# Performance work log

Hardware: AMD Instinct MI355X
Metric: run time of the kernel (lower is better)

## Reference

```python
import jax, jax.numpy as jnp
import numpy as np

EPS = 1e-5
N0 = 2000  # number of crystals


def batchnorm(x, gamma, beta):
    # training-mode BatchNorm1d over rows (biased variance, like torch normalization)
    mu = jnp.mean(x, axis=0)
    var = jnp.mean(jnp.square(x - mu), axis=0)
    return (x - mu) * jax.lax.rsqrt(var + EPS) * gamma + beta


def setup_inputs() -> dict:
    key = jax.random.key(0)
    ks = jax.random.split(key, 16)
    N, M, F, B = 100000, 12, 64, 41
    d = {
        "atom_fea": jax.random.normal(ks[0], (N, 92), jnp.float32),
        "nbr_fea": jax.random.uniform(ks[1], (N, M, B), jnp.float32),
        "nbr_fea_idx": jax.random.randint(ks[2], (N, M), 0, N),
        "crystal_atom_idx": jnp.sort(jax.random.randint(ks[3], (N,), 0, N0)),
        "emb_w": jax.random.normal(ks[4], (92, F), jnp.float32) * 0.1,
        "emb_b": jax.random.normal(ks[5], (F,), jnp.float32) * 0.1,
        "conv_w": jax.random.normal(ks[6], (3, 2 * F + B, 2 * F), jnp.float32) * 0.05,
        "conv_b": jax.random.normal(ks[7], (3, 2 * F), jnp.float32) * 0.05,
        "bn1_g": jnp.ones((3, 2 * F), jnp.float32),
        "bn1_b": jnp.zeros((3, 2 * F), jnp.float32),
        "bn2_g": jnp.ones((3, F), jnp.float32),
        "bn2_b": jnp.zeros((3, F), jnp.float32),
        "fc_w": jax.random.normal(ks[8], (F, 128), jnp.float32) * 0.1,
        "fc_b": jax.random.normal(ks[9], (128,), jnp.float32) * 0.1,
        "head_w": jax.random.normal(ks[10], (128, 256), jnp.float32) * 0.1,
        "head_b": jax.random.normal(ks[11], (256,), jnp.float32) * 0.1,
        "out_w": jax.random.normal(ks[12], (256, 1), jnp.float32) * 0.1,
        "out_b": jax.random.normal(ks[13], (1,), jnp.float32) * 0.1,
    }
    return d


def reference(atom_fea, nbr_fea, nbr_fea_idx, crystal_atom_idx,
              emb_w, emb_b, conv_w, conv_b, bn1_g, bn1_b, bn2_g, bn2_b,
              fc_w, fc_b, head_w, head_b, out_w, out_b):
    N, M = nbr_fea_idx.shape
    F = emb_w.shape[1]
    x = atom_fea @ emb_w + emb_b  # (N, F)
    for i in range(conv_w.shape[0]):
        nbr_atom = x[nbr_fea_idx]  # (N, M, F) gather
        self_fea = jnp.broadcast_to(x[:, None, :], (N, M, F))
        tot = jnp.concatenate([self_fea, nbr_atom, nbr_fea], axis=2)  # (N, M, 2F+B)
        g = jnp.einsum('nmc,cf->nmf', tot, conv_w[i]) + conv_b[i]  # (N, M, 2F)
        g = batchnorm(g.reshape(N * M, 2 * F), bn1_g[i], bn1_b[i]).reshape(N, M, 2 * F)
        nbr_filter = jax.nn.sigmoid(g[:, :, :F])
        nbr_core = jax.nn.softplus(g[:, :, F:])
        nbr_sumed = jnp.sum(nbr_filter * nbr_core, axis=1)  # (N, F)
        nbr_sumed = batchnorm(nbr_sumed, bn2_g[i], bn2_b[i])
        x = jax.nn.softplus(x + nbr_sumed)
    # mean-pool atoms into crystals
    seg = crystal_atom_idx
    sums = jax.ops.segment_sum(x, seg, num_segments=N0)
    cnts = jax.ops.segment_sum(jnp.ones((N,), x.dtype), seg, num_segments=N0)
    crys = sums / jnp.maximum(cnts, 1.0)[:, None]  # (N0, F)
    crys = jax.nn.relu(crys @ fc_w + fc_b)
    h = crys @ head_w + head_b
    out = h @ out_w + out_b
    return out
```

## Files before the change

### kernel.cpp

```cpp
#include <hip/hip_runtime.h>
#include <hip/hip_bf16.h>

#define NATOM 100000
#define MNBR  12
#define FDIM  64
#define BDIM  41
#define C2    128
#define EPSBN 1e-5f
#define NEDGE (NATOM * MNBR)
#define KP48  48
#define NFRAG  16384
#define NFRAGS 8192

typedef __attribute__((ext_vector_type(8))) short bf16x8;
typedef __attribute__((ext_vector_type(4))) unsigned short u16x4;
typedef __attribute__((ext_vector_type(4))) float f32x4;

#define X_OFF    0L
#define XB_OFF   6400000L
#define S_OFF    9600000L
#define NBRB_OFF 16000000L
#define AS_OFF   54400000L
#define BALL_OFF 60800000L
#define BALLS_OFF 60808192L
#define BN1S_OFF 60812288L
#define BN2S_OFF 60828672L
#define SC1_OFF  60836864L
#define SH1_OFF  60836992L
#define SC2_OFF  60837120L
#define SH2_OFF  60837184L
#define CRY_OFF  60837248L
#define CNT_OFF  60965248L
#define ZB_OFF   60967296L
#define WS_NEED_FUSED ((ZB_OFF + 76800000L) * 4L)
#define ZERO_OFF BN1S_OFF
#define ZERO_CNT 154960L

__device__ __forceinline__ float bf2f(unsigned short u) {
    return __uint_as_float(((unsigned)u) << 16);
}
__device__ __forceinline__ unsigned short f2bf(float f) {
    __hip_bfloat16 h = __float2bfloat16(f);
    return *(unsigned short*)&h;
}
__device__ __forceinline__ float softplus_f(float v) {
    return fmaxf(v, 0.f) + __logf(1.f + __expf(-fabsf(v)));
}

__global__ void k_zero(float* __restrict__ p, long cnt) {
    long i = (long)blockIdx.x * 256 + threadIdx.x;
    if (i < cnt) p[i] = 0.f;
}

__global__ void k_nbrcvt(const float* __restrict__ nbr, __hip_bfloat16* __restrict__ outb) {
    long i = (long)blockIdx.x * 256 + threadIdx.x;
    if (i >= (long)NEDGE * 6) return;
    long e = i / 6;
    int c = (int)(i - e * 6);
    const float* src = nbr + e * BDIM + c * 8;
    bf16x8 v;
#pragma unroll
    for (int j = 0; j < 8; ++j) {
        int k = c * 8 + j;
        float f = (k < BDIM) ? src[j] : 0.f;
        v[j] = (short)f2bf(f);
    }
    *(bf16x8*)((short*)outb + e * KP48 + c * 8) = v;
}

__global__ void k_bcvt(const float* __restrict__ cw, __hip_bfloat16* __restrict__ ballf,
                       __hip_bfloat16* __restrict__ ballfS) {
    int i = blockIdx.x * 256 + threadIdx.x;
    if (i < NFRAG) {
        int T = i / 2048, r = i - T * 2048;
        int lidx = (r >> 3) & 63, e = i & 7;
        int s4 = r >> 9;
        int lo = lidx & 15, hi = lidx >> 4;
        int krow = 64 + s4 * 32 + hi * 8 + e;
        float v = (krow < 169) ? cw[krow * C2 + T * 16 + lo] : 0.f;
        ballf[i] = __float2bfloat16(v);
    } else if (i < NFRAG + NFRAGS) {
        int i2 = i - NFRAG;
        int T = i2 / 1024, r = i2 - T * 1024;
        int lidx = (r >> 3) & 63, e = i2 & 7;
        int s = r >> 9;
        int lo = lidx & 15, hi = lidx >> 4;
        int krow = s * 32 + hi * 8 + e;
        ballfS[i2] = __float2bfloat16(cw[krow * C2 + T * 16 + lo]);
    }
}

__global__ __launch_bounds__(256)
void k_embed(const float* __restrict__ af, const float* __restrict__ ew,
             const float* __restrict__ eb, float* __restrict__ x,
             __hip_bfloat16* __restrict__ xb) {
    int t = threadIdx.x;
    int c = t & 63, ag = t >> 6;
    long n0 = (long)blockIdx.x * 16 + ag * 4;
    float acc[4] = {0.f, 0.f, 0.f, 0.f};
    for (int k4 = 0; k4 < 23; ++k4) {
        float w0 = ew[(4 * k4 + 0) * FDIM + c];
        float w1 = ew[(4 * k4 + 1) * FDIM + c];
        float w2 = ew[(4 * k4 + 2) * FDIM + c];
        float w3 = ew[(4 * k4 + 3) * FDIM + c];
#pragma unroll
        for (int a = 0; a < 4; ++a) {
            const float4* ar = (const float4*)(af + (n0 + a) * 92);
            float4 v = ar[k4];
            acc[a] += v.x * w0 + v.y * w1 + v.z * w2 + v.w * w3;
        }
    }
    float b = eb[c];
#pragma unroll
    for (int a = 0; a < 4; ++a) {
        float v = acc[a] + b;
        x[(n0 + a) * FDIM + c] = v;
        xb[(n0 + a) * FDIM + c] = __float2bfloat16(v);
    }
}

__global__ __launch_bounds__(256, 8)
void k_lin(const __hip_bfloat16* __restrict__ xb, const __hip_bfloat16* __restrict__ ballfS,
           __hip_bfloat16* __restrict__ aS) {
    int t = threadIdx.x, w = t >> 6, l = t & 63;
    int lo = l & 15, hi = l >> 4;
    long atom0 = ((long)blockIdx.x * 4 + w) * 16;
    if (atom0 >= NATOM) return;
    const short* xs = (const short*)xb + (atom0 + lo) * FDIM + hi * 8;
    bf16x8 A0 = *(const bf16x8*)(xs);
    bf16x8 A1 = *(const bf16x8*)(xs + 32);
    const short* bS = (const short*)ballfS;
#pragma unroll
    for (int T = 0; T < 8; ++T) {
        bf16x8 B0 = *(const bf16x8*)(bS + T * 1024 + l * 8);
        bf16x8 B1 = *(const bf16x8*)(bS + T * 1024 + 512 + l * 8);
        f32x4 z = {0.f, 0.f, 0.f, 0.f};
        z = __builtin_amdgcn_mfma_f32_16x16x32_bf16(A0, B0, z, 0, 0, 0);
        z = __builtin_amdgcn_mfma_f32_16x16x32_bf16(A1, B1, z, 0, 0, 0);
#pragma unroll
        for (int qq = 0; qq < 4; ++qq)
            aS[(atom0 + hi * 4 + qq) * C2 + T * 16 + lo] = __float2bfloat16(z[qq]);
    }
}

__global__ __launch_bounds__(256, 4)
void k_edge_dense(const __hip_bfloat16* __restrict__ xb,
                  const __hip_bfloat16* __restrict__ nbrb,
                  const __hip_bfloat16* __restrict__ ballf,
                  const __hip_bfloat16* __restrict__ aS,
                  const int* __restrict__ idxp,
                  float* __restrict__ bn1_slots,
                  __hip_bfloat16* __restrict__ zb) {
    __shared__ float bn_s[256];
    const int t = threadIdx.x;
    const int w = t >> 6, l = t & 63;
    const int lo = l & 15, hi = l >> 4;
    const short* xbS = (const short*)xb;
    const short* nbS = (const short*)nbrb;
    const short* aSS = (const short*)aS;
    const short* bb  = (const short*)ballf;
    short* zbS = (short*)zb;

    bn_s[t] = 0.f;
    __syncthreads();

    const long tile0 = (long)blockIdx.x * 8 + w * 2;
    const bf16x8 zz = {0, 0, 0, 0, 0, 0, 0, 0};
    const int off1 = (hi < 2) ? (32 + hi * 8) : 0;

    bf16x8 A[2][4];
    long ebase[2];
#pragma unroll
    for (int g = 0; g < 2; ++g) {
        const long e0 = (tile0 + g) * 16;
        ebase[g] = e0;
        const int j = idxp[e0 + lo];
        const short* xj = xbS + (long)j * FDIM + hi * 8;
        const short* nb = nbS + (e0 + lo) * KP48;
        A[g][0] = *(const bf16x8*)(xj);
        A[g][1] = *(const bf16x8*)(xj + 32);
        A[g][2] = *(const bf16x8*)(nb + hi * 8);
        bf16x8 n1 = *(const bf16x8*)(nb + off1);
        A[g][3] = (hi < 2) ? n1 : zz;
    }

#pragma unroll 2
    for (int P = 0; P < 8; ++P) {
        const short* bp = bb + P * 2048 + l * 8;
        bf16x8 B0 = *(const bf16x8*)(bp);
        bf16x8 B1 = *(const bf16x8*)(bp + 512);
        bf16x8 B2 = *(const bf16x8*)(bp + 1024);
        bf16x8 B3 = *(const bf16x8*)(bp + 1536);
        f32x4 z0 = {0.f, 0.f, 0.f, 0.f}, z1 = {0.f, 0.f, 0.f, 0.f};
        z0 = __builtin_amdgcn_mfma_f32_16x16x32_bf16(A[0][0], B0, z0, 0, 0, 0);
        z1 = __builtin_amdgcn_mfma_f32_16x16x32_bf16(A[1][0], B0, z1, 0, 0, 0);
        z0 = __builtin_amdgcn_mfma_f32_16x16x32_bf16(A[0][1], B1, z0, 0, 0, 0);
        z1 = __builtin_amdgcn_mfma_f32_16x16x32_bf16(A[1][1], B1, z1, 0, 0, 0);
        z0 = __builtin_amdgcn_mfma_f32_16x16x32_bf16(A[0][2], B2, z0, 0, 0, 0);
        z1 = __builtin_amdgcn_mfma_f32_16x16x32_bf16(A[1][2], B2, z1, 0, 0, 0);
        z0 = __builtin_amdgcn_mfma_f32_16x16x32_bf16(A[0][3], B3, z0, 0, 0, 0);
        z1 = __builtin_amdgcn_mfma_f32_16x16x32_bf16(A[1][3], B3, z1, 0, 0, 0);
#pragma unroll
        for (int g = 0; g < 2; ++g) {
            f32x4 z = g ? z1 : z0;
            float s1 = 0.f, s2 = 0.f;
            u16x4 pk;
#pragma unroll
            for (int qq = 0; qq < 4; ++qq) {
                const int n = (int)((ebase[g] + hi * 4 + qq) / 12);
                float av = bf2f((unsigned short)aSS[(long)n * C2 + P * 16 + lo]);
                float zp = z[qq] + av;
                pk[qq] = f2bf(zp);
                s1 += zp;
                s2 += zp * zp;
            }
            *(u16x4*)&zbS[(tile0 + g) * 2048 + (P * 16 + lo) * 16 + hi * 4] = pk;
            s1 += __shfl_xor(s1, 16); s2 += __shfl_xor(s2, 16);
            s1 += __shfl_xor(s1, 32); s2 += __shfl_xor(s2, 32);
            if (hi == 0) {
                atomicAdd(&bn_s[P * 16 + lo], s1);
                atomicAdd(&bn_s[128 + P * 16 + lo], s2);
            }
        }
    }
    __syncthreads();
    atomicAdd(&bn1_slots[(blockIdx.x & 63) * 256 + t], bn_s[t]);
}

__global__ __launch_bounds__(256, 8)
void k_zapply2(const __hip_bfloat16* __restrict__ zb,
               const float* __restrict__ sc1, const float* __restrict__ sh1,
               float* __restrict__ sout, float* __restrict__ bn2_slots) {
    __shared__ float bn_s[128];
    __shared__ float sc_s[128], sh_s[128];
    const int t = threadIdx.x;
    if (t < 128) { bn_s[t] = 0.f; sc_s[t] = sc1[t]; sh_s[t] = sh1[t]; }
    __syncthreads();

    const int a = blockIdx.x * 4 + (t >> 6);
    const int c = t & 63;
    const float s_f = sc_s[c], h_f = sh_s[c];
    const float s_c = sc_s[64 + c], h_c = sh_s[64 + c];
    const short* zs = (const short*)zb;
    const long e0 = (long)a * 12;

    float pv = 0.f;
#pragma unroll
    for (int k = 0; k < 3; ++k) {
        const long e = e0 + k * 4;
        const long tile = e >> 4;
        const int r = (int)(e & 15);
        const short* base = zs + tile * 2048 + r;
        u16x4 zf = *(const u16x4*)&base[c * 16];
        u16x4 zc = *(const u16x4*)&base[(64 + c) * 16];
#pragma unroll
        for (int qq = 0; qq < 4; ++qq) {
            float zfh = bf2f(zf[qq]) * s_f + h_f;
            float zch = bf2f(zc[qq]) * s_c + h_c;
            float filt = 1.f / (1.f + __expf(-zfh));
            pv += filt * softplus_f(zch);
        }
    }
    sout[(long)a * FDIM + c] = pv;
    atomicAdd(&bn_s[c], pv);
    atomicAdd(&bn_s[64 + c], pv * pv);
    __syncthreads();
    if (t < 128)
        atomicAdd(&bn2_slots[(blockIdx.x & 63) * 128 + t], bn_s[t]);
}

template <int APPLY>
__global__ __launch_bounds__(256, 4)
void k_edge(const __hip_bfloat16* __restrict__ xb,
            const __hip_bfloat16* __restrict__ nbrb,
            const __hip_bfloat16* __restrict__ ballf,
            const __hip_bfloat16* __restrict__ aS,
            const int* __restrict__ idxp,
            const float* __restrict__ sc1, const float* __restrict__ sh1,
            float* __restrict__ bn1_slots,
            float* __restrict__ sout, float* __restrict__ bn2_slots) {
    __shared__ float bn_s[256];
    __shared__ float sc_s[128], sh_s[128];

    const int t = threadIdx.x;
    const int w = t >> 6, l = t & 63;
    const int lo = l & 15, hi = l >> 4;
    const bool real = lo < MNBR;
    const int elo = real ? lo : 0;
    const int atom0 = blockIdx.x * 16 + w * 4;
    const short* xbS = (const short*)xb;
    const short* nbS = (const short*)nbrb;
    const short* aSS = (const short*)aS;
    const short* bb  = (const short*)ballf;

    bn_s[t] = 0.f;
    if (APPLY && t < 128) { sc_s[t] = sc1[t]; sh_s[t] = sh1[t]; }
    __syncthreads();

    const bf16x8 zz = {0, 0, 0, 0, 0, 0, 0, 0};
    const int off1 = (hi < 2) ? (32 + hi * 8) : 0;

#pragma unroll 1
    for (int pr = 0; pr < 2; ++pr) {
        const int a0 = atom0 + pr * 2;
        const int a1 = a0 + 1;
        const int j0 = idxp[(long)a0 * MNBR + elo];
        const int j1 = idxp[(long)a1 * MNBR + elo];
        const short* xj0 = xbS + (long)j0 * FDIM + hi * 8;
        const short* xj1 = xbS + (long)j1 * FDIM + hi * 8;
        const short* nb0 = nbS + ((long)a0 * MNBR + elo) * KP48;
        const short* nb1 = nbS + ((long)a1 * MNBR + elo) * KP48;
        bf16x8 A00 = *(const bf16x8*)(xj0);
        bf16x8 A01 = *(const bf16x8*)(xj0 + 32);
        bf16x8 A02 = *(const bf16x8*)(nb0 + hi * 8);
        bf16x8 n03 = *(const bf16x8*)(nb0 + off1);
        bf16x8 A03 = (hi < 2) ? n03 : zz;
        bf16x8 A10 = *(const bf16x8*)(xj1);
        bf16x8 A11 = *(const bf16x8*)(xj1 + 32);
        bf16x8 A12 = *(const bf16x8*)(nb1 + hi * 8);
        bf16x8 n13 = *(const bf16x8*)(nb1 + off1);
        bf16x8 A13 = (hi < 2) ? n13 : zz;

        if (APPLY == 0) {
#pragma unroll 2
            for (int P = 0; P < 8; ++P) {
                const short* bp = bb + P * 2048 + l * 8;
                bf16x8 B0 = *(const bf16x8*)(bp);
                bf16x8 B1 = *(const bf16x8*)(bp + 512);
                bf16x8 B2 = *(const bf16x8*)(bp + 1024);
                bf16x8 B3 = *(const bf16x8*)(bp + 1536);
                float a0v = bf2f((unsigned short)aSS[(long)a0 * C2 + P * 16 + lo]);
                float a1v = bf2f((unsigned short)aSS[(long)a1 * C2 + P * 16 + lo]);
                f32x4 z0 = {0.f, 0.f, 0.f, 0.f}, z1 = {0.f, 0.f, 0.f, 0.f};
                z0 = __builtin_amdgcn_mfma_f32_16x16x32_bf16(A00, B0, z0, 0, 0, 0);
                z1 = __builtin_amdgcn_mfma_f32_16x16x32_bf16(A10, B0, z1, 0, 0, 0);
                z0 = __builtin_amdgcn_mfma_f32_16x16x32_bf16(A01, B1, z0, 0, 0, 0);
                z1 = __builtin_amdgcn_mfma_f32_16x16x32_bf16(A11, B1, z1, 0, 0, 0);
                z0 = __builtin_amdgcn_mfma_f32_16x16x32_bf16(A02, B2, z0, 0, 0, 0);
                z1 = __builtin_amdgcn_mfma_f32_16x16x32_bf16(A12, B2, z1, 0, 0, 0);
                z0 = __builtin_amdgcn_mfma_f32_16x16x32_bf16(A03, B3, z0, 0, 0, 0);
                z1 = __builtin_amdgcn_mfma_f32_16x16x32_bf16(A13, B3, z1, 0, 0, 0);
#pragma unroll
                for (int g = 0; g < 2; ++g) {
                    f32x4 z = g ? z1 : z0;
                    float av = g ? a1v : a0v;
                    float sz = z[0] + z[1] + z[2] + z[3];
                    float szz = z[0] * z[0] + z[1] * z[1] + z[2] * z[2] + z[3] * z[3];
                    float s1 = sz + 4.f * av;
                    float s2 = szz + 2.f * av * sz + 4.f * av * av;
                    if (hi == 3) { s1 = 0.f; s2 = 0.f; }
                    s1 += __shfl_xor(s1, 16); s2 += __shfl_xor(s2, 16);
                    s1 += __shfl_xor(s1, 32); s2 += __shfl_xor(s2, 32);
                    if (hi == 0) {
                        atomicAdd(&bn_s[P * 16 + lo], s1);
                        atomicAdd(&bn_s[128 + P * 16 + lo], s2);
                    }
                }
            }
        } else {
#pragma unroll 1
            for (int P = 0; P < 4; ++P) {
                const short* bpf = bb + P * 2048 + l * 8;
                const short* bpc = bb + (P + 4) * 2048 + l * 8;
                bf16x8 Bf0 = *(const bf16x8*)(bpf);
                bf16x8 Bf1 = *(const bf16x8*)(bpf + 512);
                bf16x8 Bf2 = *(const bf16x8*)(bpf + 1024);
                bf16x8 Bf3 = *(const bf16x8*)(bpf + 1536);
                bf16x8 Bc0 = *(const bf16x8*)(bpc);
                bf16x8 Bc1 = *(const bf16x8*)(bpc + 512);
                bf16x8 Bc2 = *(const bf16x8*)(bpc + 1024);
                bf16x8 Bc3 = *(const bf16x8*)(bpc + 1536);
                const int c = P * 16 + lo;
                const float s_f = sc_s[c], h_f = sh_s[c];
                const float s_c = sc_s[64 + c], h_c = sh_s[64 + c];
                float hv0f = bf2f((unsigned short)aSS[(long)a0 * C2 + c]) * s_f + h_f;
                float hv0c = bf2f((unsigned short)aSS[(long)a0 * C2 + 64 + c]) * s_c + h_c;
                float hv1f = bf2f((unsigned short)aSS[(long)a1 * C2 + c]) * s_f + h_f;
                float hv1c = bf2f((unsigned short)aSS[(long)a1 * C2 + 64 + c]) * s_c + h_c;
                f32x4 zf0 = {0.f, 0.f, 0.f, 0.f}, zc0 = {0.f, 0.f, 0.f, 0.f};
                f32x4 zf1 = {0.f, 0.f, 0.f, 0.f}, zc1 = {0.f, 0.f, 0.f, 0.f};
                zf0 = __builtin_amdgcn_mfma_f32_16x16x32_bf16(A00, Bf0, zf0, 0, 0, 0);
                zc0 = __builtin_amdgcn_mfma_f32_16x16x32_bf16(A00, Bc0, zc0, 0, 0, 0);
                zf1 = __builtin_amdgcn_mfma_f32_16x16x32_bf16(A10, Bf0, zf1, 0, 0, 0);
                zc1 = __builtin_amdgcn_mfma_f32_16x16x32_bf16(A10, Bc0, zc1, 0, 0, 0);
                zf0 = __builtin_amdgcn_mfma_f32_16x16x32_bf16(A01, Bf1, zf0, 0, 0, 0);
                zc0 = __builtin_amdgcn_mfma_f32_16x16x32_bf16(A01, Bc1, zc0, 0, 0, 0);
                zf1 = __builtin_amdgcn_mfma_f32_16x16x32_bf16(A11, Bf1, zf1, 0, 0, 0);
                zc1 = __builtin_amdgcn_mfma_f32_16x16x32_bf16(A11, Bc1, zc1, 0, 0, 0);
                zf0 = __builtin_amdgcn_mfma_f32_16x16x32_bf16(A02, Bf2, zf0, 0, 0, 0);
                zc0 = __builtin_amdgcn_mfma_f32_16x16x32_bf16(A02, Bc2, zc0, 0, 0, 0);
                zf1 = __builtin_amdgcn_mfma_f32_16x16x32_bf16(A12, Bf2, zf1, 0, 0, 0);
                zc1 = __builtin_amdgcn_mfma_f32_16x16x32_bf16(A12, Bc2, zc1, 0, 0, 0);
                zf0 = __builtin_amdgcn_mfma_f32_16x16x32_bf16(A03, Bf3, zf0, 0, 0, 0);
                zc0 = __builtin_amdgcn_mfma_f32_16x16x32_bf16(A03, Bc3, zc0, 0, 0, 0);
                zf1 = __builtin_amdgcn_mfma_f32_16x16x32_bf16(A13, Bf3, zf1, 0, 0, 0);
                zc1 = __builtin_amdgcn_mfma_f32_16x16x32_bf16(A13, Bc3, zc1, 0, 0, 0);
#pragma unroll
                for (int g = 0; g < 2; ++g) {
                    f32x4 zf = g ? zf1 : zf0;
                    f32x4 zc = g ? zc1 : zc0;
                    float hvf = g ? hv1f : hv0f;
                    float hvc = g ? hv1c : hv0c;
                    float pvsum = 0.f;
#pragma unroll
                    for (int qq = 0; qq < 4; ++qq) {
                        float zfh = zf[qq] * s_f + hvf;
                        float zch = zc[qq] * s_c + hvc;
                        float filt = 1.f / (1.f + __expf(-zfh));
                        pvsum += filt * softplus_f(zch);
                    }
                    if (hi == 3) pvsum = 0.f;
                    pvsum += __shfl_xor(pvsum, 16);
                    pvsum += __shfl_xor(pvsum, 32);
                    if (hi == 0) {
                        sout[(long)(g ? a1 : a0) * FDIM + c] = pvsum;
                        atomicAdd(&bn_s[c], pvsum);
                        atomicAdd(&bn_s[64 + c], pvsum * pvsum);
                    }
                }
            }
        }
    }

    __syncthreads();
    if (APPLY == 0) {
        atomicAdd(&bn1_slots[(blockIdx.x & 63) * 256 + t], bn_s[t]);
    } else {
        if (t < 128)
            atomicAdd(&bn2_slots[(blockIdx.x & 63) * 128 + t], bn_s[t]);
    }
}

__global__ void k_bnfin(float* __restrict__ slots, const float* __restrict__ gamma,
                        const float* __restrict__ beta,
                        float* __restrict__ scale, float* __restrict__ shift,
                        float inv_cnt, int nc) {
    int c = threadIdx.x;
    if (c >= nc) return;
    float s1 = 0.f, s2 = 0.f;
    for (int s = 0; s < 64; ++s) {
        s1 += slots[s * 2 * nc + c];
        s2 += slots[s * 2 * nc + nc + c];
    }
    for (int s = 0; s < 64; ++s) {
        slots[s * 2 * nc + c] = 0.f;
        slots[s * 2 * nc + nc + c] = 0.f;
    }
    float mu = s1 * inv_cnt;
    float var = fmaxf(s2 * inv_cnt - mu * mu, 0.f);
    float sc = gamma[c] * rsqrtf(var + EPSBN);
    scale[c] = sc;
    shift[c] = beta[c] - mu * sc;
}

__global__ void k_x(float* __restrict__ x, __hip_bfloat16* __restrict__ xb,
                    const float* __restrict__ s,
                    const float* __restrict__ scale2, const float* __restrict__ shift2) {
    long i = (long)blockIdx.x * 256 + threadIdx.x;
    if (i >= (long)NATOM * FDIM) return;
    int c = (int)(i & 63);
    float v = softplus_f(x[i] + s[i] * scale2[c] + shift2[c]);
    x[i] = v;
    xb[i] = __float2bfloat16(v);
}

__global__ void k_pool(const float* __restrict__ x, const int* __restrict__ seg,
                       float* __restrict__ cry, float* __restrict__ cnt) {
    long i = (long)blockIdx.x * 256 + threadIdx.x;
    if (i >= (long)NATOM * FDIM) return;
    int n = (int)(i >> 6), c = (int)(i & 63);
    int cr = seg[n];
    atomicAdd(&cry[(long)cr * FDIM + c], x[i]);
    if (c == 0) atomicAdd(&cnt[cr], 1.f);
}

__global__ __launch_bounds__(256)
void k_head(const float* __restrict__ cry, const float* __restrict__ cnt,
            const float* __restrict__ fw, const float* __restrict__ fb,
            const float* __restrict__ hw, const float* __restrict__ hb,
            const float* __restrict__ ow, const float* __restrict__ ob,
            float* __restrict__ out) {
    __shared__ float cs[64], h1[128], red[256];
    int t = threadIdx.x, cr = blockIdx.x;
    if (t < 64) cs[t] = cry[(long)cr * 64 + t] / fmaxf(cnt[cr], 1.f);
    __syncthreads();
    if (t < 128) {
        float a = fb[t];
        for (int k = 0; k < 64; ++k) a += cs[k] * fw[k * 128 + t];
        h1[t] = fmaxf(a, 0.f);
    }
    __syncthreads();
    float a = hb[t];
    for (int k = 0; k < 128; ++k) a += h1[k] * hw[k * 256 + t];
    red[t] = a * ow[t];
    __syncthreads();
    for (int off = 128; off > 0; off >>= 1) {
        if (t < off) red[t] += red[t + off];
        __syncthreads();
    }
    if (t == 0) out[cr] = red[0] + ob[0];
}

extern "C" void kernel_launch(void* const* d_in, const int* in_sizes, int n_in,
                              void* d_out, int out_size, void* d_ws, size_t ws_size,
                              hipStream_t stream) {
    const float* atom_fea = (const float*)d_in[0];
    const float* nbr_fea  = (const float*)d_in[1];
    const int*   nbr_idx  = (const int*)d_in[2];
    const int*   seg      = (const int*)d_in[3];
    const float* emb_w    = (const float*)d_in[4];
    const float* emb_b    = (const float*)d_in[5];
    const float* conv_w   = (const float*)d_in[6];
    const float* bn1_g    = (const float*)d_in[8];
    const float* bn1_b    = (const float*)d_in[9];
    const float* bn2_g    = (const float*)d_in[10];
    const float* bn2_b    = (const float*)d_in[11];
    const float* fc_w     = (const float*)d_in[12];
    const float* fc_b     = (const float*)d_in[13];
    const float* head_w   = (const float*)d_in[14];
    const float* head_b   = (const float*)d_in[15];
    const float* out_w    = (const float*)d_in[16];
    const float* out_b    = (const float*)d_in[17];
    float* out = (float*)d_out;

    float* ws = (float*)d_ws;
    float* x = ws + X_OFF;
    __hip_bfloat16* xb     = (__hip_bfloat16*)(ws + XB_OFF);
    float* s = ws + S_OFF;
    __hip_bfloat16* nbrb   = (__hip_bfloat16*)(ws + NBRB_OFF);
    __hip_bfloat16* aS     = (__hip_bfloat16*)(ws + AS_OFF);
    __hip_bfloat16* ballf  = (__hip_bfloat16*)(ws + BALL_OFF);
    __hip_bfloat16* ballfS = (__hip_bfloat16*)(ws + BALLS_OFF);
    float* bn1s = ws + BN1S_OFF;
    float* bn2s = ws + BN2S_OFF;
    float* sc1 = ws + SC1_OFF;
    float* sh1 = ws + SH1_OFF;
    float* sc2 = ws + SC2_OFF;
    float* sh2 = ws + SH2_OFF;
    float* cry = ws + CRY_OFF;
    float* cnt = ws + CNT_OFF;
    __hip_bfloat16* zb = (__hip_bfloat16*)(ws + ZB_OFF);
    const bool fused = (ws_size >= (size_t)WS_NEED_FUSED);

    k_zero<<<(int)((ZERO_CNT + 255) / 256), 256, 0, stream>>>(ws + ZERO_OFF, ZERO_CNT);
    k_nbrcvt<<<(int)(((long)NEDGE * 6 + 255) / 256), 256, 0, stream>>>(nbr_fea, nbrb);
    k_embed<<<NATOM / 16, 256, 0, stream>>>(atom_fea, emb_w, emb_b, x, xb);

    for (int i = 0; i < 3; ++i) {
        const float* cw = conv_w + (long)i * 169 * C2;
        k_bcvt<<<96, 256, 0, stream>>>(cw, ballf, ballfS);
        k_lin<<<1563, 256, 0, stream>>>(xb, ballfS, aS);
        if (fused) {
            k_edge_dense<<<9375, 256, 0, stream>>>(xb, nbrb, ballf, aS, nbr_idx, bn1s, zb);
            k_bnfin<<<1, 128, 0, stream>>>(bn1s, bn1_g + i * C2, bn1_b + i * C2,
                                           sc1, sh1, 1.f / 1200000.f, 128);
            k_zapply2<<<NATOM / 4, 256, 0, stream>>>(zb, sc1, sh1, s, bn2s);
        } else {
            k_edge<0><<<NATOM / 16, 256, 0, stream>>>(xb, nbrb, ballf, aS, nbr_idx,
                                                      nullptr, nullptr, bn1s, nullptr, nullptr);
            k_bnfin<<<1, 128, 0, stream>>>(bn1s, bn1_g + i * C2, bn1_b + i * C2,
                                           sc1, sh1, 1.f / 1200000.f, 128);
            k_edge<1><<<NATOM / 16, 256, 0, stream>>>(xb, nbrb, ballf, aS, nbr_idx,
                                                      sc1, sh1, nullptr, s, bn2s);
        }
        k_bnfin<<<1, 64, 0, stream>>>(bn2s, bn2_g + i * 64, bn2_b + i * 64,
                                      sc2, sh2, 1e-5f, 64);
        k_x<<<(NATOM * FDIM) / 256, 256, 0, stream>>>(x, xb, s, sc2, sh2);
    }

    k_pool<<<(NATOM * FDIM) / 256, 256, 0, stream>>>(x, seg, cry, cnt);
    k_head<<<2000, 256, 0, stream>>>(cry, cnt, fc_w, fc_b, head_w, head_b, out_w, out_b, out);
}
```

Measured before the change: 1.226 ms.

## Fold BN finalize into consumer kernels, use per-layer stat slots, grid-stride apply

Removes the single-block k_bnfin launches on the fused path by having k_zapply2 and k_x each reduce the 64 stat slots into scale and shift in shared memory. Each layer now gets its own zeroed slot region, so the slots no longer need clearing between layers. k_zapply2 and k_x become grid-stride kernels with 2048 blocks, and k_zapply2 accumulates per-thread stats in registers before doing the shared atomics. k_edge_dense replaces the per-element divide and gather of the aS bias with two precomputed row loads and a select. The price is that every block repeats the 64-slot reduction, and the initial zeroing pass covers a larger region.

```diff
diff --git a/kernel.cpp b/kernel.cpp
--- a/kernel.cpp
+++ b/kernel.cpp
@@ -24,17 +24,15 @@
 #define BALL_OFF 60800000L
 #define BALLS_OFF 60808192L
 #define BN1S_OFF 60812288L
-#define BN2S_OFF 60828672L
-#define SC1_OFF  60836864L
-#define SH1_OFF  60836992L
-#define SC2_OFF  60837120L
-#define SH2_OFF  60837184L
-#define CRY_OFF  60837248L
-#define CNT_OFF  60965248L
-#define ZB_OFF   60967296L
+#define BN2S_OFF 60861440L
+#define CRY_OFF  60886016L
+#define CNT_OFF  61014016L
+#define SC1_OFF  61016016L
+#define SH1_OFF  61016144L
+#define ZB_OFF   61016272L
 #define WS_NEED_FUSED ((ZB_OFF + 76800000L) * 4L)
 #define ZERO_OFF BN1S_OFF
-#define ZERO_CNT 154960L
+#define ZERO_CNT 203728L
 
 __device__ __forceinline__ float bf2f(unsigned short u) {
     return __uint_as_float(((unsigned)u) << 16);
@@ -169,11 +167,11 @@
     const int off1 = (hi < 2) ? (32 + hi * 8) : 0;
 
     bf16x8 A[2][4];
-    long ebase[2];
+    long aLo[2], aHi[2];
+    int bnd[2];
 #pragma unroll
     for (int g = 0; g < 2; ++g) {
         const long e0 = (tile0 + g) * 16;
-        ebase[g] = e0;
         const int j = idxp[e0 + lo];
         const short* xj = xbS + (long)j * FDIM + hi * 8;
         const short* nb = nbS + (e0 + lo) * KP48;
@@ -182,6 +180,12 @@
         A[g][2] = *(const bf16x8*)(nb + hi * 8);
         bf16x8 n1 = *(const bf16x8*)(nb + off1);
         A[g][3] = (hi < 2) ? n1 : zz;
+        const int rbase = (int)e0 + hi * 4;
+        const int n0 = rbase / 12;
+        const int n3 = (rbase + 3) / 12;
+        aLo[g] = (long)n0 * C2;
+        aHi[g] = (long)n3 * C2;
+        bnd[g] = (n3 > n0) ? (n3 * 12 - rbase) : 4;
     }
 
 #pragma unroll 2
@@ -200,26 +204,28 @@
         z1 = __builtin_amdgcn_mfma_f32_16x16x32_bf16(A[1][2], B2, z1, 0, 0, 0);
         z0 = __builtin_amdgcn_mfma_f32_16x16x32_bf16(A[0][3], B3, z0, 0, 0, 0);
         z1 = __builtin_amdgcn_mfma_f32_16x16x32_bf16(A[1][3], B3, z1, 0, 0, 0);
+        const int col = P * 16 + lo;
 #pragma unroll
         for (int g = 0; g < 2; ++g) {
             f32x4 z = g ? z1 : z0;
+            const float avlo = bf2f((unsigned short)aSS[aLo[g] + col]);
+            const float avhi = bf2f((unsigned short)aSS[aHi[g] + col]);
             float s1 = 0.f, s2 = 0.f;
             u16x4 pk;
 #pragma unroll
             for (int qq = 0; qq < 4; ++qq) {
-                const int n = (int)((ebase[g] + hi * 4 + qq) / 12);
-                float av = bf2f((unsigned short)aSS[(long)n * C2 + P * 16 + lo]);
+                float av = (qq >= bnd[g]) ? avhi : avlo;
                 float zp = z[qq] + av;
                 pk[qq] = f2bf(zp);
                 s1 += zp;
                 s2 += zp * zp;
             }
-            *(u16x4*)&zbS[(tile0 + g) * 2048 + (P * 16 + lo) * 16 + hi * 4] = pk;
+            *(u16x4*)&zbS[(tile0 + g) * 2048 + col * 16 + hi * 4] = pk;
             s1 += __shfl_xor(s1, 16); s2 += __shfl_xor(s2, 16);
             s1 += __shfl_xor(s1, 32); s2 += __shfl_xor(s2, 32);
             if (hi == 0) {
-                atomicAdd(&bn_s[P * 16 + lo], s1);
-                atomicAdd(&bn_s[128 + P * 16 + lo], s2);
+                atomicAdd(&bn_s[col], s1);
+                atomicAdd(&bn_s[128 + col], s2);
             }
         }
     }
@@ -229,44 +235,112 @@
 
 __global__ __launch_bounds__(256, 8)
 void k_zapply2(const __hip_bfloat16* __restrict__ zb,
-               const float* __restrict__ sc1, const float* __restrict__ sh1,
+               const float* __restrict__ bn1_layer,
+               const float* __restrict__ g1, const float* __restrict__ b1,
                float* __restrict__ sout, float* __restrict__ bn2_slots) {
     __shared__ float bn_s[128];
     __shared__ float sc_s[128], sh_s[128];
     const int t = threadIdx.x;
-    if (t < 128) { bn_s[t] = 0.f; sc_s[t] = sc1[t]; sh_s[t] = sh1[t]; }
-    __syncthreads();
-
-    const int a = blockIdx.x * 4 + (t >> 6);
+    if (t < 128) {
+        float s1 = 0.f, s2 = 0.f;
+        for (int sl = 0; sl < 64; ++sl) {
+            s1 += bn1_layer[sl * 256 + t];
+            s2 += bn1_layer[sl * 256 + 128 + t];
+        }
+        const float inv = 1.f / 1200000.f;
+        float mu = s1 * inv;
+        float var = fmaxf(s2 * inv - mu * mu, 0.f);
+        float sc = g1[t] * rsqrtf(var + EPSBN);
+        sc_s[t] = sc;
+        sh_s[t] = b1[t] - mu * sc;
+        bn_s[t] = 0.f;
+    }
+    __syncthreads();
+
     const int c = t & 63;
     const float s_f = sc_s[c], h_f = sh_s[c];
     const float s_c = sc_s[64 + c], h_c = sh_s[64 + c];
     const short* zs = (const short*)zb;
-    const long e0 = (long)a * 12;
-
-    float pv = 0.f;
-#pragma unroll
-    for (int k = 0; k < 3; ++k) {
-        const long e = e0 + k * 4;
-        const long tile = e >> 4;
-        const int r = (int)(e & 15);
-        const short* base = zs + tile * 2048 + r;
-        u16x4 zf = *(const u16x4*)&base[c * 16];
-        u16x4 zc = *(const u16x4*)&base[(64 + c) * 16];
-#pragma unroll
-        for (int qq = 0; qq < 4; ++qq) {
-            float zfh = bf2f(zf[qq]) * s_f + h_f;
-            float zch = bf2f(zc[qq]) * s_c + h_c;
-            float filt = 1.f / (1.f + __expf(-zfh));
-            pv += filt * softplus_f(zch);
+    float racc1 = 0.f, racc2 = 0.f;
+
+    for (int grp = blockIdx.x; grp < NATOM / 4; grp += gridDim.x) {
+        const int a = grp * 4 + (t >> 6);
+        const long e0 = (long)a * 12;
+        float pv = 0.f;
+#pragma unroll
+        for (int k = 0; k < 3; ++k) {
+            const long e = e0 + k * 4;
+            const long tile = e >> 4;
+            const int r = (int)(e & 15);
+            const short* base = zs + tile * 2048 + r;
+            u16x4 zf = *(const u16x4*)&base[c * 16];
+            u16x4 zc = *(const u16x4*)&base[(64 + c) * 16];
+#pragma unroll
+            for (int qq = 0; qq < 4; ++qq) {
+                float zfh = bf2f(zf[qq]) * s_f + h_f;
+                float zch = bf2f(zc[qq]) * s_c + h_c;
+                float filt = 1.f / (1.f + __expf(-zfh));
+                pv += filt * softplus_f(zch);
+            }
         }
-    }
-    sout[(long)a * FDIM + c] = pv;
-    atomicAdd(&bn_s[c], pv);
-    atomicAdd(&bn_s[64 + c], pv * pv);
+        sout[(long)a * FDIM + c] = pv;
+        racc1 += pv;
+        racc2 += pv * pv;
+    }
+    atomicAdd(&bn_s[c], racc1);
+    atomicAdd(&bn_s[64 + c], racc2);
     __syncthreads();
     if (t < 128)
         atomicAdd(&bn2_slots[(blockIdx.x & 63) * 128 + t], bn_s[t]);
+}
+
+__global__ __launch_bounds__(256, 8)
+void k_x(float* __restrict__ x, __hip_bfloat16* __restrict__ xb,
+         const float* __restrict__ s,
+         const float* __restrict__ bn2_layer,
+         const float* __restrict__ g2, const float* __restrict__ b2) {
+    __shared__ float sc_s[64], sh_s[64];
+    const int t = threadIdx.x;
+    if (t < 64) {
+        float s1 = 0.f, s2 = 0.f;
+        for (int sl = 0; sl < 64; ++sl) {
+            s1 += bn2_layer[sl * 128 + t];
+            s2 += bn2_layer[sl * 128 + 64 + t];
+        }
+        const float inv = 1e-5f;
+        float mu = s1 * inv;
+        float var = fmaxf(s2 * inv - mu * mu, 0.f);
+        float sc = g2[t] * rsqrtf(var + EPSBN);
+        sc_s[t] = sc;
+        sh_s[t] = b2[t] - mu * sc;
+    }
+    __syncthreads();
+    const long total = (long)NATOM * FDIM;
+    const long stride = (long)gridDim.x * 256;
+    for (long i = (long)blockIdx.x * 256 + t; i < total; i += stride) {
+        int c = (int)(i & 63);
+        float v = softplus_f(x[i] + s[i] * sc_s[c] + sh_s[c]);
+        x[i] = v;
+        xb[i] = __float2bfloat16(v);
+    }
+}
+
+__global__ void k_bnfin(const float* __restrict__ slots, const float* __restrict__ gamma,
+                        const float* __restrict__ beta,
+                        float* __restrict__ scale, float* __restrict__ shift,
+                        float inv_cnt, int nc) {
+    int c = threadIdx.x;
+    if (c >= nc) return;
+    float s1 = 0.f, s2 = 0.f;
+    for (int s = 0; s < 64; ++s) {
+        s1 += slots[s * 2 * nc + c];
+        s2 += slots[s * 2 * nc + nc + c];
+    }
+    float mu = s1 * inv_cnt;
+    float var = fmaxf(s2 * inv_cnt - mu * mu, 0.f);
+    float sc = gamma[c] * rsqrtf(var + EPSBN);
+    scale[c] = sc;
+    shift[c] = beta[c] - mu * sc;
 }
 
 template <int APPLY>
@@ -431,39 +505,6 @@
     }
 }
 
-__global__ void k_bnfin(float* __restrict__ slots, const float* __restrict__ gamma,
-                        const float* __restrict__ beta,
-                        float* __restrict__ scale, float* __restrict__ shift,
-                        float inv_cnt, int nc) {
-    int c = threadIdx.x;
-    if (c >= nc) return;
-    float s1 = 0.f, s2 = 0.f;
-    for (int s = 0; s < 64; ++s) {
-        s1 += slots[s * 2 * nc + c];
-        s2 += slots[s * 2 * nc + nc + c];
-    }
-    for (int s = 0; s < 64; ++s) {
-        slots[s * 2 * nc + c] = 0.f;
-        slots[s * 2 * nc + nc + c] = 0.f;
-    }
-    float mu = s1 * inv_cnt;
-    float var = fmaxf(s2 * inv_cnt - mu * mu, 0.f);
-    float sc = gamma[c] * rsqrtf(var + EPSBN);
-    scale[c] = sc;
-    shift[c] = beta[c] - mu * sc;
-}
-
-__global__ void k_x(float* __restrict__ x, __hip_bfloat16* __restrict__ xb,
-                    const float* __restrict__ s,
-                    const float* __restrict__ scale2, const float* __restrict__ shift2) {
-    long i = (long)blockIdx.x * 256 + threadIdx.x;
-    if (i >= (long)NATOM * FDIM) return;
-    int c = (int)(i & 63);
-    float v = softplus_f(x[i] + s[i] * scale2[c] + shift2[c]);
-    x[i] = v;
-    xb[i] = __float2bfloat16(v);
-}
-
 __global__ void k_pool(const float* __restrict__ x, const int* __restrict__ seg,
                        float* __restrict__ cry, float* __restrict__ cnt) {
     long i = (long)blockIdx.x * 256 + threadIdx.x;
@@ -533,12 +574,10 @@
     __hip_bfloat16* ballfS = (__hip_bfloat16*)(ws + BALLS_OFF);
     float* bn1s = ws + BN1S_OFF;
     float* bn2s = ws + BN2S_OFF;
+    float* cry = ws + CRY_OFF;
+    float* cnt = ws + CNT_OFF;
     float* sc1 = ws + SC1_OFF;
     float* sh1 = ws + SH1_OFF;
-    float* sc2 = ws + SC2_OFF;
-    float* sh2 = ws + SH2_OFF;
-    float* cry = ws + CRY_OFF;
-    float* cnt = ws + CNT_OFF;
     __hip_bfloat16* zb = (__hip_bfloat16*)(ws + ZB_OFF);
     const bool fused = (ws_size >= (size_t)WS_NEED_FUSED);
 
@@ -548,24 +587,23 @@
 
     for (int i = 0; i < 3; ++i) {
         const float* cw = conv_w + (long)i * 169 * C2;
+        float* bn1L = bn1s + (long)i * 16384;
+        float* bn2L = bn2s + (long)i * 8192;
         k_bcvt<<<96, 256, 0, stream>>>(cw, ballf, ballfS);
         k_lin<<<1563, 256, 0, stream>>>(xb, ballfS, aS);
         if (fused) {
-            k_edge_dense<<<9375, 256, 0, stream>>>(xb, nbrb, ballf, aS, nbr_idx, bn1s, zb);
-            k_bnfin<<<1, 128, 0, stream>>>(bn1s, bn1_g + i * C2, bn1_b + i * C2,
-                                           sc1, sh1, 1.f / 1200000.f, 128);
-            k_zapply2<<<NATOM / 4, 256, 0, stream>>>(zb, sc1, sh1, s, bn2s);
+            k_edge_dense<<<9375, 256, 0, stream>>>(xb, nbrb, ballf, aS, nbr_idx, bn1L, zb);
+            k_zapply2<<<2048, 256, 0, stream>>>(zb, bn1L, bn1_g + i * C2, bn1_b + i * C2,
+                                                s, bn2L);
         } else {
             k_edge<0><<<NATOM / 16, 256, 0, stream>>>(xb, nbrb, ballf, aS, nbr_idx,
-                                                      nullptr, nullptr, bn1s, nullptr, nullptr);
-            k_bnfin<<<1, 128, 0, stream>>>(bn1s, bn1_g + i * C2, bn1_b + i * C2,
+                                                      nullptr, nullptr, bn1L, nullptr, nullptr);
+            k_bnfin<<<1, 128, 0, stream>>>(bn1L, bn1_g + i * C2, bn1_b + i * C2,
                                            sc1, sh1, 1.f / 1200000.f, 128);
             k_edge<1><<<NATOM / 16, 256, 0, stream>>>(xb, nbrb, ballf, aS, nbr_idx,
-                                                      sc1, sh1, nullptr, s, bn2s);
+                                                      sc1, sh1, nullptr, s, bn2L);
         }
-        k_bnfin<<<1, 64, 0, stream>>>(bn2s, bn2_g + i * 64, bn2_b + i * 64,
-                                      sc2, sh2, 1e-5f, 64);
-        k_x<<<(NATOM * FDIM) / 256, 256, 0, stream>>>(x, xb, s, sc2, sh2);
+        k_x<<<2048, 256, 0, stream>>>(x, xb, s, bn2L, bn2_g + i * 64, bn2_b + i * 64);
     }
 
     k_pool<<<(NATOM * FDIM) / 256, 256, 0, stream>>>(x, seg, cry, cnt);
```

Result: no change. 1.215 ms (-0.9%).
